# Kernel optimization log

Hardware: AMD Instinct MI355X
Metric: run time of the kernel (lower is better)

Reference implementation:

```python
import jax, jax.numpy as jnp
import numpy as np
import math

L = 2          # n_layers
H = 12         # n_heads
D = 768        # hidden_size
S = 2048       # seq_len
BS = 128       # block_size
HALO = 32      # halo_size
INNER = 3072   # inner_size
EPS = 1e-12    # layer_norm_eps
DH = D // H    # head dim
NB = S // BS   # num blocks
WIN = BS + 2 * HALO  # key/value window per block


def _layer_norm(x, g, b):
    mu = jnp.mean(x, axis=-1, keepdims=True)
    var = jnp.mean(jnp.square(x - mu), axis=-1, keepdims=True)
    return (x - mu) * jax.lax.rsqrt(var + EPS) * g + b


def setup_inputs() -> dict:
    key = jax.random.key(0)
    ks = jax.random.split(key, 20)
    s = 0.02
    inp = {"x": jax.random.normal(ks[0], (8, S, D), jnp.float32)}
    # stacked per-layer params [L, ...]
    inp["Wq"] = jax.random.normal(ks[1], (L, D, D)) * s
    inp["bq"] = jnp.zeros((L, D))
    inp["Wk"] = jax.random.normal(ks[2], (L, D, D)) * s
    inp["bk"] = jnp.zeros((L, D))
    inp["Wv"] = jax.random.normal(ks[3], (L, D, D)) * s
    inp["bv"] = jnp.zeros((L, D))
    inp["Wo"] = jax.random.normal(ks[4], (L, D, D)) * s
    inp["bo"] = jnp.zeros((L, D))
    inp["ln1_g"] = jnp.ones((L, D))
    inp["ln1_b"] = jnp.zeros((L, D))
    inp["W1"] = jax.random.normal(ks[5], (L, D, INNER)) * s
    inp["b1"] = jnp.zeros((L, INNER))
    inp["W2"] = jax.random.normal(ks[6], (L, INNER, D)) * s
    inp["b2"] = jnp.zeros((L, D))
    inp["ln2_g"] = jnp.ones((L, D))
    inp["ln2_b"] = jnp.zeros((L, D))
    return inp


def _halo_layer(x, Wq, bq, Wk, bk, Wv, bv, Wo, bo, ln1_g, ln1_b, W1, b1, W2, b2, ln2_g, ln2_b):
    B = x.shape[0]
    # --- block-local halo attention (vectorized over blocks) ---
    # window gather via zero-padding + masking: padded positions are masked
    # to -inf in scores, which is mathematically identical to the original
    # smaller windows at the first/last block.
    xp = jnp.pad(x, ((0, 0), (HALO, HALO), (0, 0)))          # [B, S+2h, D]
    idx = (jnp.arange(NB) * BS)[:, None] + jnp.arange(WIN)[None, :]
    valid = ((idx - HALO) >= 0) & ((idx - HALO) < S)
    xw = xp[:, idx]

    q = (x @ Wq + bq).reshape(B, NB, BS, H, DH)
    k = (xw @ Wk + bk).reshape(B, NB, WIN, H, DH)
    v = (xw @ Wv + bv).reshape(B, NB, WIN, H, DH)

    scores = jnp.einsum('bnqhd,bnkhd->bnhqk', q, k) / math.sqrt(DH)
    neg = jnp.finfo(scores.dtype).min
    scores = jnp.where(valid[None, :, None, None, :], scores, neg)
    probs = jax.nn.softmax(scores, axis=-1)
    ctx = jnp.einsum('bnhqk,bnkhd->bnqhd', probs, v).reshape(B, S, D)

    attn_out = _layer_norm(ctx @ Wo + bo + x, ln1_g, ln1_b)

    # --- feed forward (gelu, exact erf form as torch default) ---
    h = jax.nn.gelu(attn_out @ W1 + b1, approximate=False)
    h = h @ W2 + b2
    return _layer_norm(h + attn_out, ln2_g, ln2_b)


def reference(x, Wq, bq, Wk, bk, Wv, bv, Wo, bo, ln1_g, ln1_b,
              W1, b1, W2, b2, ln2_g, ln2_b):
    outs = []
    h = x
    for l in range(L):
        h = _halo_layer(h, Wq[l], bq[l], Wk[l], bk[l], Wv[l], bv[l], Wo[l], bo[l],
                        ln1_g[l], ln1_b[l], W1[l], b1[l], W2[l], b2[l], ln2_g[l], ln2_b[l])
        outs.append(h)
    return jnp.stack(outs)  # [L, B, S, D] == list of all encoded layers
```

## Files before the change

kernel.cpp:

```cpp
#include <hip/hip_runtime.h>
#include <hip/hip_bf16.h>

typedef unsigned short u16;
typedef unsigned int u32;

static const int DD = 768;
static const int SS = 2048;
static const int BB = 8;
static const int HH = 12;
static const int NBLK = 16;
static const int ROWS = BB * SS;
static const size_t AD = (size_t)ROWS * DD;
static const size_t D2 = (size_t)DD * DD;
static const size_t DI = (size_t)DD * 3072;

typedef __attribute__((ext_vector_type(8))) short short8;
typedef __attribute__((ext_vector_type(4))) float f32x4;

union U16x8 { uint4 u; short8 s; };

__device__ __forceinline__ float bl(u32 u) { return __uint_as_float(u << 16); }
__device__ __forceinline__ float bh(u32 u) { return __uint_as_float(u & 0xffff0000u); }
__device__ __forceinline__ u16 f2b(float f) {
    u32 u = __float_as_uint(f);
    u += 0x7fffu + ((u >> 16) & 1u);
    return (u16)(u >> 16);
}
__device__ __forceinline__ u32 pack2(float lo, float hi) {
    return (u32)f2b(lo) | ((u32)f2b(hi) << 16);
}

__device__ __forceinline__ void gload16(const u16* g, u16* l) {
    __builtin_amdgcn_global_load_lds(
        (const __attribute__((address_space(1))) void*)g,
        (__attribute__((address_space(3))) void*)l, 16, 0, 0);
}

__global__ __launch_bounds__(256) void cast_bf16(const float* __restrict__ x,
                                                 u16* __restrict__ xb, int n) {
    int i = (blockIdx.x * 256 + threadIdx.x) * 4;
    if (i < n) {
        float4 v = *reinterpret_cast<const float4*>(x + i);
        uint2 p;
        p.x = pack2(v.x, v.y);
        p.y = pack2(v.z, v.w);
        *reinterpret_cast<uint2*>(xb + i) = p;
    }
}

__global__ __launch_bounds__(256) void cast_transpose(const float* __restrict__ W,
                                                      u16* __restrict__ WT,
                                                      int K, int N) {
    __shared__ float tile[32][33];
    int bx = blockIdx.x;
    int by = blockIdx.y;
    int tx = threadIdx.x;
    int ty = threadIdx.y;
#pragma unroll
    for (int i = 0; i < 4; i++) {
        int kr = by * 32 + ty + i * 8;
        tile[ty + i * 8][tx] = W[(size_t)kr * N + bx * 32 + tx];
    }
    __syncthreads();
#pragma unroll
    for (int i = 0; i < 4; i++) {
        int nr = bx * 32 + ty + i * 8;
        WT[(size_t)nr * K + by * 32 + tx] = f2b(tile[tx][ty + i * 8]);
    }
}

template <int EPI>
__global__ __launch_bounds__(256) void gemm128(const u16* __restrict__ A,
                                               const u16* __restrict__ BT,
                                               const float* __restrict__ b0,
                                               const float* __restrict__ b1,
                                               const float* __restrict__ b2,
                                               void* __restrict__ C0,
                                               void* __restrict__ C1,
                                               void* __restrict__ C2,
                                               int M, int N, int K, int NTN) {
    extern __shared__ u16 smem[];
    const int tid = threadIdx.x;
    const int nwg = gridDim.x;
    int wg = blockIdx.x;
    wg = (wg & 7) * (nwg >> 3) + (wg >> 3);
    const int tn = wg % NTN, tm = wg / NTN;
    const int m0 = tm * 128, n0 = tn * 128;
    const int lane = tid & 63, w = tid >> 6;
    const int wr = w >> 1, wc = w & 1;
    const int lr = lane & 15, ls = lane >> 4;

    const int r3 = tid >> 2, c2 = tid & 3;
    const int kswz = ((c2 ^ (r3 & 3)) << 3);
    const u16* gA = A + (size_t)(m0 + r3) * K + kswz;
    const u16* gB = BT + (size_t)(n0 + r3) * K + kswz;
    const size_t rstep = (size_t)64 * K;

    f32x4 acc[4][4];
#pragma unroll
    for (int i = 0; i < 4; i++)
#pragma unroll
        for (int j = 0; j < 4; j++) acc[i][j] = (f32x4){0.f, 0.f, 0.f, 0.f};

    const int NT = K >> 5;
    {
        u16* pA = smem + tid * 8;
        u16* pB = smem + 4096 + tid * 8;
#pragma unroll
        for (int j = 0; j < 2; j++) {
            gload16(gA + j * rstep, pA + j * 2048);
            gload16(gB + j * rstep, pB + j * 2048);
        }
    }
    __syncthreads();

    for (int t = 0; t < NT; ++t) {
        if (t + 1 < NT) {
            const int nb = (t + 1) & 1;
            u16* pA = smem + nb * 8192 + tid * 8;
            u16* pB = smem + nb * 8192 + 4096 + tid * 8;
            const u16* sA = gA + (size_t)(t + 1) * 32;
            const u16* sB = gB + (size_t)(t + 1) * 32;
#pragma unroll
            for (int j = 0; j < 2; j++) {
                gload16(sA + j * rstep, pA + j * 2048);
                gload16(sB + j * rstep, pB + j * 2048);
            }
        }
        const u16* bufA = smem + (t & 1) * 8192 + (wr * 64 + lr) * 32;
        const u16* bufB = smem + (t & 1) * 8192 + 4096 + (wc * 64 + lr) * 32;
        const int sl = ls ^ (lr & 3);
        U16x8 af[4], bf[4];
#pragma unroll
        for (int ni = 0; ni < 4; ni++)
            bf[ni].u = *(const uint4*)(bufB + ni * 512 + sl * 8);
#pragma unroll
        for (int mi = 0; mi < 4; mi++)
            af[mi].u = *(const uint4*)(bufA + mi * 512 + sl * 8);
#pragma unroll
        for (int mi = 0; mi < 4; mi++)
#pragma unroll
            for (int ni = 0; ni < 4; ni++)
                acc[mi][ni] = __builtin_amdgcn_mfma_f32_16x16x32_bf16(
                    af[mi].s, bf[ni].s, acc[mi][ni], 0, 0, 0);
        __syncthreads();
    }

#pragma unroll
    for (int mi = 0; mi < 4; mi++) {
        int row0 = m0 + wr * 64 + mi * 16 + ls * 4;
#pragma unroll
        for (int ni = 0; ni < 4; ni++) {
            int col = n0 + wc * 64 + ni * 16 + lr;
            float v[4];
            if (EPI == 4) {
                int band = col / 768;
                int colq = col - band * 768;
                const float* bp = (band == 0) ? b0 : (band == 1) ? b1 : b2;
                float bs = bp[colq];
#pragma unroll
                for (int r = 0; r < 4; r++) v[r] = acc[mi][ni][r] + bs;
                if (band == 2) {
                    uint2 wv;
                    wv.x = pack2(v[0], v[1]);
                    wv.y = pack2(v[2], v[3]);
                    *reinterpret_cast<uint2*>((u16*)C2 + (size_t)colq * M + row0) = wv;
                } else {
                    u16* dst = (band == 0) ? (u16*)C0 : (u16*)C1;
#pragma unroll
                    for (int r = 0; r < 4; r++)
                        dst[(size_t)(row0 + r) * 768 + colq] = f2b(v[r]);
                }
            } else {
                float bs = b0[col];
#pragma unroll
                for (int r = 0; r < 4; r++) {
                    v[r] = acc[mi][ni][r] + bs;
                    if (EPI == 2) v[r] = 0.5f * v[r] * (1.0f + erff(v[r] * 0.70710678118654752f));
                }
                if (EPI == 1) {
#pragma unroll
                    for (int r = 0; r < 4; r++)
                        ((float*)C0)[(size_t)(row0 + r) * N + col] = v[r];
                } else {
#pragma unroll
                    for (int r = 0; r < 4; r++)
                        ((u16*)C0)[(size_t)(row0 + r) * N + col] = f2b(v[r]);
                }
            }
        }
    }
}

__global__ __launch_bounds__(256) void resid_ln(const float* __restrict__ a,
                                                const float* __restrict__ res,
                                                const float* __restrict__ g,
                                                const float* __restrict__ be,
                                                float* __restrict__ of,
                                                u16* __restrict__ ob) {
    __shared__ float red[8];
    const int row = blockIdx.x;
    const int tid = threadIdx.x;
    const size_t base = (size_t)row * 768;
    float v[3];
    float s = 0.f;
#pragma unroll
    for (int i = 0; i < 3; i++) {
        int c = tid + i * 256;
        v[i] = a[base + c] + res[base + c];
        s += v[i];
    }
#pragma unroll
    for (int off = 32; off; off >>= 1) s += __shfl_down(s, off);
    if ((tid & 63) == 0) red[tid >> 6] = s;
    __syncthreads();
    float mean = (red[0] + red[1] + red[2] + red[3]) * (1.f / 768.f);
    float q = 0.f;
#pragma unroll
    for (int i = 0; i < 3; i++) {
        float d = v[i] - mean;
        q += d * d;
    }
#pragma unroll
    for (int off = 32; off; off >>= 1) q += __shfl_down(q, off);
    if ((tid & 63) == 0) red[4 + (tid >> 6)] = q;
    __syncthreads();
    float var = (red[4] + red[5] + red[6] + red[7]) * (1.f / 768.f);
    float inv = rsqrtf(var + 1e-12f);
#pragma unroll
    for (int i = 0; i < 3; i++) {
        int c = tid + i * 256;
        float y = (v[i] - mean) * inv * g[c] + be[c];
        of[base + c] = y;
        ob[base + c] = f2b(y);
    }
}

__global__ __launch_bounds__(256) void attn_mfma(const u16* __restrict__ Q,
                                                 const u16* __restrict__ Kx,
                                                 const u16* __restrict__ Vt,
                                                 u16* __restrict__ Ctx) {
    __shared__ u16 sm0[128 * 104];
    __shared__ u16 sm1[64 * 192];
    u16* Ks = sm0;
    u16* Ps = sm0;
    u16* Vs = sm1;

    const int bid = blockIdx.x;
    const int h = bid % HH;
    const int n = (bid / HH) % NBLK;
    const int b = bid / (HH * NBLK);
    const int tid = threadIdx.x;
    const int lane = tid & 63, w = tid >> 6;
    const int lr = lane & 15, ls = lane >> 4;
    const int s0 = n * 128 - 32;

#pragma unroll
    for (int j = 0; j < 6; j++) {
        int r = (tid >> 3) + j * 32;
        int c = tid & 7;
        int s = min(max(s0 + r, 0), SS - 1);
        uint4 kv = *reinterpret_cast<const uint4*>(Kx + ((size_t)(b * SS + s)) * 768 + h * 64 + c * 8);
        int byteo = r * 128 + ((c * 16) ^ ((r & 7) << 4));
        *reinterpret_cast<uint4*>(Ks + (byteo >> 1)) = kv;
    }
#pragma unroll
    for (int j = 0; j < 6; j++) {
        int d = tid >> 2;
        int c = (tid & 3) + j * 4;
        int sv = min(max(s0 + c * 8, 0), SS - 8);
        uint4 vv = *reinterpret_cast<const uint4*>(Vt + ((size_t)(h * 64 + d)) * ROWS + b * SS + sv);
        int byteo = d * 384 + ((c * 16) ^ ((d & 7) << 4));
        *reinterpret_cast<uint4*>(Vs + (byteo >> 1)) = vv;
    }
    __syncthreads();

    const int qrow0 = b * SS + n * 128 + w * 32;
    U16x8 qf[2][2];
#pragma unroll
    for (int mi = 0; mi < 2; mi++)
#pragma unroll
        for (int ks = 0; ks < 2; ks++)
            qf[mi][ks].u = *reinterpret_cast<const uint4*>(
                Q + (size_t)(qrow0 + mi * 16 + lr) * 768 + h * 64 + ks * 32 + ls * 8);

    f32x4 sc[2][12];
#pragma unroll
    for (int mi = 0; mi < 2; mi++)
#pragma unroll
        for (int jt = 0; jt < 12; jt++) sc[mi][jt] = (f32x4){0.f, 0.f, 0.f, 0.f};
#pragma unroll
    for (int jt = 0; jt < 12; jt++) {
        U16x8 kf[2];
#pragma unroll
        for (int ks = 0; ks < 2; ks++) {
            int r = jt * 16 + lr;
            int byteo = r * 128 + ((ks * 64 + ls * 16) ^ ((r & 7) << 4));
            kf[ks].u = *reinterpret_cast<const uint4*>(Ks + (byteo >> 1));
        }
#pragma unroll
        for (int mi = 0; mi < 2; mi++)
#pragma unroll
            for (int ks = 0; ks < 2; ks++)
                sc[mi][jt] = __builtin_amdgcn_mfma_f32_16x16x32_bf16(
                    qf[mi][ks].s, kf[ks].s, sc[mi][jt], 0, 0, 0);
    }

    const int lo = (n == 0) ? 32 : 0;
    const int hi = (n == NBLK - 1) ? 160 : 192;
    float mx[2][4], sm[2][4], inv[2][4];
#pragma unroll
    for (int mi = 0; mi < 2; mi++)
#pragma unroll
        for (int r = 0; r < 4; r++) { mx[mi][r] = -3.0e38f; sm[mi][r] = 0.f; }
#pragma unroll
    for (int jt = 0; jt < 12; jt++) {
        int col = jt * 16 + lr;
        bool valid = (col >= lo) && (col < hi);
#pragma unroll
        for (int mi = 0; mi < 2; mi++)
#pragma unroll
            for (int r = 0; r < 4; r++) {
                float v = valid ? sc[mi][jt][r] * 0.125f : -3.0e38f;
                sc[mi][jt][r] = v;
                mx[mi][r] = fmaxf(mx[mi][r], v);
            }
    }
#pragma unroll
    for (int o = 1; o <= 8; o <<= 1)
#pragma unroll
        for (int mi = 0; mi < 2; mi++)
#pragma unroll
            for (int r = 0; r < 4; r++)
                mx[mi][r] = fmaxf(mx[mi][r], __shfl_xor(mx[mi][r], o));
#pragma unroll
    for (int jt = 0; jt < 12; jt++)
#pragma unroll
        for (int mi = 0; mi < 2; mi++)
#pragma unroll
            for (int r = 0; r < 4; r++) {
                float p = __expf(sc[mi][jt][r] - mx[mi][r]);
                sc[mi][jt][r] = p;
                sm[mi][r] += p;
            }
#pragma unroll
    for (int o = 1; o <= 8; o <<= 1)
#pragma unroll
        for (int mi = 0; mi < 2; mi++)
#pragma unroll
            for (int r = 0; r < 4; r++)
                sm[mi][r] += __shfl_xor(sm[mi][r], o);
#pragma unroll
    for (int mi = 0; mi < 2; mi++)
#pragma unroll
        for (int r = 0; r < 4; r++) inv[mi][r] = 1.0f / sm[mi][r];

    f32x4 oacc[2][4];
#pragma unroll
    for (int mi = 0; mi < 2; mi++)
#pragma unroll
        for (int dt = 0; dt < 4; dt++) oacc[mi][dt] = (f32x4){0.f, 0.f, 0.f, 0.f};
    __syncthreads();

#pragma unroll
    for (int ph = 0; ph < 2; ph++) {
#pragma unroll
        for (int jj = 0; jj < 6; jj++) {
            int jt = ph * 6 + jj;
#pragma unroll
            for (int mi = 0; mi < 2; mi++) {
                int row = w * 32 + mi * 16 + ls * 4;
#pragma unroll
                for (int r = 0; r < 4; r++)
                    Ps[(row + r) * 104 + jj * 16 + lr] = f2b(sc[mi][jt][r]);
            }
        }
        __syncthreads();
#pragma unroll
        for (int kk = 0; kk < 3; kk++) {
            U16x8 pf[2], vf[4];
#pragma unroll
            for (int mi = 0; mi < 2; mi++)
                pf[mi].u = *reinterpret_cast<const uint4*>(
                    Ps + (w * 32 + mi * 16 + lr) * 104 + kk * 32 + ls * 8);
#pragma unroll
            for (int dt = 0; dt < 4; dt++) {
                int rrow = dt * 16 + lr;
                int byteo = rrow * 384 + ((ph * 192 + kk * 64 + ls * 16) ^ ((rrow & 7) << 4));
                vf[dt].u = *reinterpret_cast<const uint4*>(Vs + (byteo >> 1));
            }
#pragma unroll
            for (int mi = 0; mi < 2; mi++)
#pragma unroll
                for (int dt = 0; dt < 4; dt++)
                    oacc[mi][dt] = __builtin_amdgcn_mfma_f32_16x16x32_bf16(
                        pf[mi].s, vf[dt].s, oacc[mi][dt], 0, 0, 0);
        }
        __syncthreads();
    }

#pragma unroll
    for (int mi = 0; mi < 2; mi++)
#pragma unroll
        for (int dt = 0; dt < 4; dt++)
#pragma unroll
            for (int r = 0; r < 4; r++) {
                float v = oacc[mi][dt][r] * inv[mi][r];
                Ctx[(size_t)(qrow0 + mi * 16 + ls * 4 + r) * 768 + h * 64 + dt * 16 + lr] = f2b(v);
            }
}

extern "C" void kernel_launch(void* const* d_in, const int* in_sizes, int n_in,
                              void* d_out, int out_size, void* d_ws, size_t ws_size,
                              hipStream_t stream) {
    (void)in_sizes; (void)n_in; (void)out_size; (void)ws_size;
    const float* x    = (const float*)d_in[0];
    const float* Wq   = (const float*)d_in[1];
    const float* bq   = (const float*)d_in[2];
    const float* Wk   = (const float*)d_in[3];
    const float* bk   = (const float*)d_in[4];
    const float* Wv   = (const float*)d_in[5];
    const float* bv   = (const float*)d_in[6];
    const float* Wo   = (const float*)d_in[7];
    const float* bo   = (const float*)d_in[8];
    const float* ln1g = (const float*)d_in[9];
    const float* ln1b = (const float*)d_in[10];
    const float* W1   = (const float*)d_in[11];
    const float* b1   = (const float*)d_in[12];
    const float* W2   = (const float*)d_in[13];
    const float* b2   = (const float*)d_in[14];
    const float* ln2g = (const float*)d_in[15];
    const float* ln2b = (const float*)d_in[16];
    float* out = (float*)d_out;

    char* ws = (char*)d_ws;
    size_t off = 0;
    auto alloc = [&](size_t bytes) -> char* {
        char* p = ws + off;
        off += (bytes + 255) & ~(size_t)255;
        return p;
    };
    u16* WqkvT = (u16*)alloc(2 * 3 * D2 * sizeof(u16));
    u16* WoT   = (u16*)alloc(2 * D2 * sizeof(u16));
    u16* W1T   = (u16*)alloc(2 * DI * sizeof(u16));
    u16* W2T   = (u16*)alloc(2 * DI * sizeof(u16));
    u16* Xb    = (u16*)alloc(AD * sizeof(u16));
    u16* RegA  = (u16*)alloc(4 * AD * sizeof(u16));
    float* AttnF = (float*)alloc(AD * sizeof(float));
    u16*   AttnB = (u16*)alloc(AD * sizeof(u16));
    float* H2f   = (float*)alloc(AD * sizeof(float));
    u16* Qb = RegA;
    u16* Kb = RegA + AD;
    u16* Vtb = RegA + 2 * AD;
    u16* Ctxb = RegA + 3 * AD;
    u16* H1b = RegA;

    {
        int nelem = ROWS * DD;
        cast_bf16<<<dim3(nelem / 4 / 256), dim3(256), 0, stream>>>(x, Xb, nelem);
    }
    for (int l = 0; l < 2; l++) {
        u16* base = WqkvT + (size_t)l * 3 * D2;
        cast_transpose<<<dim3(24, 24), dim3(32, 8), 0, stream>>>(Wq + l * D2, base, 768, 768);
        cast_transpose<<<dim3(24, 24), dim3(32, 8), 0, stream>>>(Wk + l * D2, base + D2, 768, 768);
        cast_transpose<<<dim3(24, 24), dim3(32, 8), 0, stream>>>(Wv + l * D2, base + 2 * D2, 768, 768);
        cast_transpose<<<dim3(24, 24), dim3(32, 8), 0, stream>>>(Wo + l * D2, WoT + l * D2, 768, 768);
        cast_transpose<<<dim3(96, 24), dim3(32, 8), 0, stream>>>(W1 + l * DI, W1T + l * DI, 768, 3072);
        cast_transpose<<<dim3(24, 96), dim3(32, 8), 0, stream>>>(W2 + l * DI, W2T + l * DI, 3072, 768);
    }

    const size_t LDSB = 32768;
    const float* xres = x;
    for (int l = 0; l < 2; l++) {
        gemm128<4><<<dim3(128 * 18), 256, LDSB, stream>>>(
            Xb, WqkvT + (size_t)l * 3 * D2, bq + l * 768, bk + l * 768, bv + l * 768,
            Qb, Kb, Vtb, ROWS, 2304, 768, 18);
        attn_mfma<<<dim3(BB * NBLK * HH), 256, 0, stream>>>(Qb, Kb, Vtb, Ctxb);
        gemm128<1><<<dim3(128 * 6), 256, LDSB, stream>>>(
            Ctxb, WoT + l * D2, bo + l * 768, nullptr, nullptr,
            H2f, nullptr, nullptr, ROWS, 768, 768, 6);
        resid_ln<<<dim3(ROWS), 256, 0, stream>>>(H2f, xres, ln1g + l * 768, ln1b + l * 768, AttnF, AttnB);
        gemm128<2><<<dim3(128 * 24), 256, LDSB, stream>>>(
            AttnB, W1T + l * DI, b1 + l * 3072, nullptr, nullptr,
            H1b, nullptr, nullptr, ROWS, 3072, 768, 24);
        gemm128<1><<<dim3(128 * 6), 256, LDSB, stream>>>(
            H1b, W2T + l * DI, b2 + l * 768, nullptr, nullptr,
            H2f, nullptr, nullptr, ROWS, 768, 3072, 6);
        float* outl = out + (size_t)l * AD;
        resid_ln<<<dim3(ROWS), 256, 0, stream>>>(H2f, AttnF, ln2g + l * 768, ln2b + l * 768, outl, Xb);
        xres = outl;
    }
}
```

Baseline: 925.6 us.

## Use triple-buffered LDS pipeline with explicit vmcnt waits in GEMM

Replaces the double-buffered LDS prefetch in the bf16 MFMA GEMM with a three-stage ring, issuing global-to-LDS loads three K-tiles ahead and waiting on vmcnt counters instead of full syncthreads. It reads fragments, barriers, then refills the just-consumed slot before running MFMAs at raised wave priority. The goal is to hide global load latency behind compute. In exchange it needs 48KB of LDS per block, which may lower occupancy, and it depends on exact vmcnt accounting from the gload16 helper.

```diff
diff --git a/kernel.cpp b/kernel.cpp
--- a/kernel.cpp
+++ b/kernel.cpp
@@ -103,32 +103,28 @@
         for (int j = 0; j < 4; j++) acc[i][j] = (f32x4){0.f, 0.f, 0.f, 0.f};
 
     const int NT = K >> 5;
-    {
-        u16* pA = smem + tid * 8;
-        u16* pB = smem + 4096 + tid * 8;
-#pragma unroll
-        for (int j = 0; j < 2; j++) {
-            gload16(gA + j * rstep, pA + j * 2048);
-            gload16(gB + j * rstep, pB + j * 2048);
-        }
-    }
-    __syncthreads();
-
+#pragma unroll
+    for (int p = 0; p < 3; ++p) {
+        u16* pA = smem + p * 8192 + tid * 8;
+        u16* pB = smem + p * 8192 + 4096 + tid * 8;
+        const u16* sA = gA + (size_t)p * 32;
+        const u16* sB = gB + (size_t)p * 32;
+        gload16(sA, pA);
+        gload16(sA + rstep, pA + 2048);
+        gload16(sB, pB);
+        gload16(sB + rstep, pB + 2048);
+    }
+
+    int slot = 0;
     for (int t = 0; t < NT; ++t) {
-        if (t + 1 < NT) {
-            const int nb = (t + 1) & 1;
-            u16* pA = smem + nb * 8192 + tid * 8;
-            u16* pB = smem + nb * 8192 + 4096 + tid * 8;
-            const u16* sA = gA + (size_t)(t + 1) * 32;
-            const u16* sB = gB + (size_t)(t + 1) * 32;
-#pragma unroll
-            for (int j = 0; j < 2; j++) {
-                gload16(sA + j * rstep, pA + j * 2048);
-                gload16(sB + j * rstep, pB + j * 2048);
-            }
-        }
-        const u16* bufA = smem + (t & 1) * 8192 + (wr * 64 + lr) * 32;
-        const u16* bufB = smem + (t & 1) * 8192 + 4096 + (wc * 64 + lr) * 32;
+        if (t + 2 < NT)      asm volatile("s_waitcnt vmcnt(8)" ::: "memory");
+        else if (t + 1 < NT) asm volatile("s_waitcnt vmcnt(4)" ::: "memory");
+        else                 asm volatile("s_waitcnt vmcnt(0)" ::: "memory");
+        __builtin_amdgcn_s_barrier();
+        __builtin_amdgcn_sched_barrier(0);
+
+        const u16* bufA = smem + slot * 8192 + (wr * 64 + lr) * 32;
+        const u16* bufB = smem + slot * 8192 + 4096 + (wc * 64 + lr) * 32;
         const int sl = ls ^ (lr & 3);
         U16x8 af[4], bf[4];
 #pragma unroll
@@ -137,13 +133,32 @@
 #pragma unroll
         for (int mi = 0; mi < 4; mi++)
             af[mi].u = *(const uint4*)(bufA + mi * 512 + sl * 8);
+        asm volatile("s_waitcnt lgkmcnt(0)" ::: "memory");
+        __builtin_amdgcn_sched_barrier(0);
+        __builtin_amdgcn_s_barrier();
+        __builtin_amdgcn_sched_barrier(0);
+
+        if (t + 3 < NT) {
+            u16* pA = smem + slot * 8192 + tid * 8;
+            u16* pB = smem + slot * 8192 + 4096 + tid * 8;
+            const u16* sA = gA + (size_t)(t + 3) * 32;
+            const u16* sB = gB + (size_t)(t + 3) * 32;
+            gload16(sA, pA);
+            gload16(sA + rstep, pA + 2048);
+            gload16(sB, pB);
+            gload16(sB + rstep, pB + 2048);
+        }
+        __builtin_amdgcn_sched_barrier(0);
+
+        __builtin_amdgcn_s_setprio(1);
 #pragma unroll
         for (int mi = 0; mi < 4; mi++)
 #pragma unroll
             for (int ni = 0; ni < 4; ni++)
                 acc[mi][ni] = __builtin_amdgcn_mfma_f32_16x16x32_bf16(
                     af[mi].s, bf[ni].s, acc[mi][ni], 0, 0, 0);
-        __syncthreads();
+        __builtin_amdgcn_s_setprio(0);
+        slot = (slot == 2) ? 0 : slot + 1;
     }
 
 #pragma unroll
@@ -469,7 +484,7 @@
         cast_transpose<<<dim3(24, 96), dim3(32, 8), 0, stream>>>(W2 + l * DI, W2T + l * DI, 3072, 768);
     }
 
-    const size_t LDSB = 32768;
+    const size_t LDSB = 49152;
     const float* xres = x;
     for (int l = 0; l < 2; l++) {
         gemm128<4><<<dim3(128 * 18), 256, LDSB, stream>>>(
```

After: 908.3 us. About the same (-1.9%).
